# Optimization experiments

Measured on AMD Instinct MI355X. Metric: run time of the kernel, lower is better.

The kernel has to match this reference:

```python
import jax, jax.numpy as jnp
import numpy as np

DIM = 512
NUM_HEADS = 8
HEAD_DIM = DIM // NUM_HEADS
SCALE = HEAD_DIM ** -0.5
B, N = 8, 1024


def setup_inputs() -> dict:
    key = jax.random.key(0)
    k1, k2, k3, k4, k5 = jax.random.split(key, 5)
    x = jax.random.normal(k1, (B, N, DIM), dtype=jnp.float32)
    rpe_bias = jax.random.normal(k2, (1, NUM_HEADS, N, N), dtype=jnp.float32)
    # torch Linear weights: [out_features, in_features], y = x @ W.T
    qkv_w = jax.random.normal(k3, (3 * DIM, DIM), dtype=jnp.float32) * (DIM ** -0.5)
    proj_w = jax.random.normal(k4, (DIM, DIM), dtype=jnp.float32) * (DIM ** -0.5)
    proj_b = jax.random.normal(k5, (DIM,), dtype=jnp.float32) * 0.01
    return {"x": x, "rpe_bias": rpe_bias, "qkv_w": qkv_w, "proj_w": proj_w, "proj_b": proj_b}


def reference(x, rpe_bias, qkv_w, proj_w, proj_b):
    b, n, c = x.shape
    h, d = NUM_HEADS, HEAD_DIM
    # qkv projection (no bias): [B,N,3C] -> [3,B,H,N,D]
    qkv = (x @ qkv_w.T).reshape(b, n, 3, h, d).transpose(2, 0, 3, 1, 4)
    q, k, v = qkv[0], qkv[1], qkv[2]
    attn = jnp.einsum('bhnd,bhmd->bhnm', q, k) * SCALE + rpe_bias
    attn = jax.nn.softmax(attn, axis=-1)  # dropout p=0 -> identity
    out = jnp.einsum('bhnm,bhmd->bhnd', attn, v)
    out = out.transpose(0, 2, 1, 3).reshape(b, n, c)
    return out @ proj_w.T + proj_b
```

## Files before the change

### kernel.cpp

```cpp
#include <hip/hip_runtime.h>
#include <hip/hip_bf16.h>

#define B_    8
#define N_    1024
#define DIM_  512
#define H_    8
#define DH_   64
#define SCALE_ 0.125f

typedef unsigned short u16;
typedef __attribute__((ext_vector_type(8))) short bf16x8;
typedef __attribute__((ext_vector_type(4))) float f32x4;

__device__ __forceinline__ u16 f2bf(float f) {
  union { float f; unsigned u; } v; v.f = f;
  return (u16)((v.u + 0x7fffu + ((v.u >> 16) & 1u)) >> 16);
}
__device__ __forceinline__ unsigned pack2(float a, float b) {
  return (unsigned)f2bf(a) | ((unsigned)f2bf(b) << 16);
}
__device__ __forceinline__ void cp16(const void* g, void* l) {
  __builtin_amdgcn_global_load_lds(
      (const __attribute__((address_space(1))) unsigned*)g,
      (__attribute__((address_space(3))) unsigned*)l, 16, 0, 0);
}

__global__ __launch_bounds__(256) void convert_kernel(
    const float* __restrict__ X, const float* __restrict__ Wq,
    const float* __restrict__ Wp, u16* __restrict__ Xb,
    u16* __restrict__ Wqb, u16* __restrict__ Wpb) {
  const int NX4 = (B_ * N_ * DIM_) / 4;
  const int NQ4 = (3 * DIM_ * DIM_) / 4;
  const int NP4 = (DIM_ * DIM_) / 4;
  const int total = NX4 + NQ4 + NP4;
  const int stride = gridDim.x * 256;
  for (int i = blockIdx.x * 256 + threadIdx.x; i < total; i += stride) {
    const float* s; u16* d; int off;
    if (i < NX4)            { s = X;  d = Xb;  off = i; }
    else if (i < NX4 + NQ4) { s = Wq; d = Wqb; off = i - NX4; }
    else                    { s = Wp; d = Wpb; off = i - NX4 - NQ4; }
    float4 f = *(const float4*)(s + (size_t)off * 4);
    uint2 u; u.x = pack2(f.x, f.y); u.y = pack2(f.z, f.w);
    *(uint2*)(d + (size_t)off * 4) = u;
  }
}

__global__ __launch_bounds__(256) void qkv_gemm(
    const u16* __restrict__ Ab, const u16* __restrict__ Bb,
    u16* __restrict__ Q, u16* __restrict__ K, u16* __restrict__ Vt) {
  __shared__ __align__(16) u16 sA[128 * 64];
  __shared__ __align__(16) u16 sB[128 * 64];
  const int t = threadIdx.x;
  const int wv = t >> 6, lane = t & 63, quad = (lane >> 4) & 3, l15 = lane & 15;
  const int wr = wv >> 1, wc = wv & 1;
  const int m0 = blockIdx.y * 128;
  const int n0 = blockIdx.x * 128;

  const int srow = lane >> 3;
  const int schunk = (lane & 7) ^ srow;
  const size_t ga = (size_t)(m0 + srow) * DIM_ + schunk * 8;
  const size_t gb = (size_t)(n0 + srow) * DIM_ + schunk * 8;

  f32x4 zero = {0.f, 0.f, 0.f, 0.f};
  f32x4 acc[4][4];
#pragma unroll
  for (int i = 0; i < 4; i++)
#pragma unroll
    for (int j = 0; j < 4; j++) acc[i][j] = zero;

  for (int k0 = 0; k0 < DIM_; k0 += 64) {
    __syncthreads();
#pragma unroll
    for (int i = 0; i < 4; i++) {
      const int rb = 32 * wv + 8 * i;
      cp16(Ab + ga + (size_t)rb * DIM_ + k0, &sA[rb * 64]);
      cp16(Bb + gb + (size_t)rb * DIM_ + k0, &sB[rb * 64]);
    }
    __syncthreads();
#pragma unroll
    for (int ks = 0; ks < 2; ks++) {
      bf16x8 af[4], bfv[4];
#pragma unroll
      for (int i = 0; i < 4; i++)
        af[i] = *(const bf16x8*)&sA[(wr * 64 + 16 * i + l15) * 64 +
                                    (((ks << 2) | quad) ^ (l15 & 7)) * 8];
#pragma unroll
      for (int j = 0; j < 4; j++)
        bfv[j] = *(const bf16x8*)&sB[(wc * 64 + 16 * j + l15) * 64 +
                                     (((ks << 2) | quad) ^ (l15 & 7)) * 8];
#pragma unroll
      for (int i = 0; i < 4; i++)
#pragma unroll
        for (int j = 0; j < 4; j++)
          acc[i][j] = __builtin_amdgcn_mfma_f32_16x16x32_bf16(af[i], bfv[j], acc[i][j], 0, 0, 0);
    }
  }

  const int tsel = n0 >> 9;
#pragma unroll
  for (int j = 0; j < 4; j++) {
    const int jg = n0 + wc * 64 + 16 * j + l15;
    const int h = (jg >> 6) & 7, d = jg & 63;
#pragma unroll
    for (int i = 0; i < 4; i++) {
      const int mbase = m0 + wr * 64 + 16 * i + quad * 4;
      const int b = mbase >> 10, nb = mbase & 1023;
      const size_t bh = (size_t)(b * H_ + h);
      if (tsel == 2) {
        ushort4 v4;
        v4.x = f2bf(acc[i][j][0]); v4.y = f2bf(acc[i][j][1]);
        v4.z = f2bf(acc[i][j][2]); v4.w = f2bf(acc[i][j][3]);
        *(ushort4*)&Vt[(bh * DH_ + d) * N_ + nb] = v4;
      } else {
        u16* dst = (tsel == 0 ? Q : K);
#pragma unroll
        for (int rr = 0; rr < 4; rr++)
          dst[(bh * N_ + nb + rr) * DH_ + d] = f2bf(acc[i][j][rr]);
      }
    }
  }
}

__global__ __launch_bounds__(256) void attn_kernel(
    const u16* __restrict__ Q, const u16* __restrict__ K,
    const u16* __restrict__ Vt, const float* __restrict__ bias,
    u16* __restrict__ AO) {
  __shared__ __align__(16) u16 sK[64 * 72];
  __shared__ __align__(16) u16 sV[64 * 72];
  __shared__ __align__(16) u16 sP[64 * 72];
  const int t = threadIdx.x;
  const int wv = t >> 6, lane = t & 63, quad = (lane >> 4) & 3, l15 = lane & 15;

  const int bid = blockIdx.x;
  const int h = bid & 7;
  const int s = bid >> 3;
  const int nx = s >> 3;
  const int b = s & 7;
  const int n0 = nx * 64;
  const int bh = b * H_ + h;
  const int r = t >> 2, c = (t & 3) << 4;

  const int qg = n0 + 16 * wv + l15;
  bf16x8 qf0, qf1;
  {
    const u16* qsrc = Q + (((size_t)bh << 10) + qg) * DH_ + (quad << 3);
    qf0 = *(const bf16x8*)qsrc;
    qf1 = *(const bf16x8*)(qsrc + 32);
  }

  const float* bp = bias + (((size_t)h << 10) + qg) * N_ + (quad << 2);
  const u16* kbase = K + (((size_t)bh << 10) + r) * DH_ + c;
  const u16* vbase = Vt + (((size_t)bh << 6) + r) * N_ + c;

  f32x4 zero = {0.f, 0.f, 0.f, 0.f};
  f32x4 O[4];
  O[0] = zero; O[1] = zero; O[2] = zero; O[3] = zero;
  float lsum = 0.f;

  uint4 kA0 = *(const uint4*)kbase, kA1 = *(const uint4*)(kbase + 8);
  uint4 vA0 = *(const uint4*)vbase, vA1 = *(const uint4*)(vbase + 8);
  uint4 kB0 = *(const uint4*)(kbase + (size_t)64 * DH_);
  uint4 kB1 = *(const uint4*)(kbase + (size_t)64 * DH_ + 8);
  uint4 vB0 = *(const uint4*)(vbase + 64), vB1 = *(const uint4*)(vbase + 72);
  float4 bA[4], bB[4];
#pragma unroll
  for (int cb = 0; cb < 4; cb++) {
    bA[cb] = *(const float4*)(bp + 16 * cb);
    bB[cb] = *(const float4*)(bp + 64 + 16 * cb);
  }

  auto tile = [&](int kt, uint4& k0r, uint4& k1r, uint4& v0r, uint4& v1r,
                  float4 (&bias4)[4]) {
    __syncthreads();
    *(uint4*)&sK[r * 72 + c] = k0r;  *(uint4*)&sK[r * 72 + c + 8] = k1r;
    *(uint4*)&sV[r * 72 + c] = v0r;  *(uint4*)&sV[r * 72 + c + 8] = v1r;
    if (kt + 2 < 16) {
      const u16* kn = kbase + (size_t)(kt + 2) * 64 * DH_;
      const u16* vn = vbase + (kt + 2) * 64;
      k0r = *(const uint4*)kn; k1r = *(const uint4*)(kn + 8);
      v0r = *(const uint4*)vn; v1r = *(const uint4*)(vn + 8);
    }
    __syncthreads();

    f32x4 S[4];
    S[0] = zero; S[1] = zero; S[2] = zero; S[3] = zero;
#pragma unroll
    for (int ks = 0; ks < 2; ks++) {
      const bf16x8 qf = ks ? qf1 : qf0;
#pragma unroll
      for (int cb = 0; cb < 4; cb++) {
        bf16x8 kf = *(const bf16x8*)&sK[(16 * cb + l15) * 72 + ks * 32 + (quad << 3)];
        S[cb] = __builtin_amdgcn_mfma_f32_16x16x32_bf16(kf, qf, S[cb], 0, 0, 0);
      }
    }

#pragma unroll
    for (int cb = 0; cb < 4; cb++) {
      float p0 = __expf(fmaf(S[cb][0], SCALE_, bias4[cb].x));
      float p1 = __expf(fmaf(S[cb][1], SCALE_, bias4[cb].y));
      float p2 = __expf(fmaf(S[cb][2], SCALE_, bias4[cb].z));
      float p3 = __expf(fmaf(S[cb][3], SCALE_, bias4[cb].w));
      lsum += (p0 + p1) + (p2 + p3);
      uint2 pk;
      pk.x = pack2(p0, p1);
      pk.y = pack2(p2, p3);
      *(uint2*)&sP[(16 * wv + l15) * 72 + 16 * cb + (quad << 2)] = pk;
    }
    if (kt + 2 < 16) {
      const float* bn = bp + (kt + 2) * 64;
#pragma unroll
      for (int cb = 0; cb < 4; cb++) bias4[cb] = *(const float4*)(bn + 16 * cb);
    }
    asm volatile("s_waitcnt lgkmcnt(0)" ::: "memory");

#pragma unroll
    for (int ks = 0; ks < 2; ks++) {
      bf16x8 pf = *(const bf16x8*)&sP[(16 * wv + l15) * 72 + ks * 32 + (quad << 3)];
#pragma unroll
      for (int cb = 0; cb < 4; cb++) {
        bf16x8 vf = *(const bf16x8*)&sV[(16 * cb + l15) * 72 + ks * 32 + (quad << 3)];
        O[cb] = __builtin_amdgcn_mfma_f32_16x16x32_bf16(vf, pf, O[cb], 0, 0, 0);
      }
    }
  };

  for (int kt = 0; kt < 16; kt += 2) {
    tile(kt, kA0, kA1, vA0, vA1, bA);
    tile(kt + 1, kB0, kB1, vB0, vB1, bB);
  }

  lsum += __shfl_xor(lsum, 16);
  lsum += __shfl_xor(lsum, 32);
  const float inv = 1.f / lsum;
#pragma unroll
  for (int cb = 0; cb < 4; cb++) {
    ushort4 o4;
    o4.x = f2bf(O[cb][0] * inv); o4.y = f2bf(O[cb][1] * inv);
    o4.z = f2bf(O[cb][2] * inv); o4.w = f2bf(O[cb][3] * inv);
    *(ushort4*)&AO[(((size_t)b << 10) + qg) * DIM_ + h * DH_ + 16 * cb + (quad << 2)] = o4;
  }
}

__global__ __launch_bounds__(256) void proj_gemm(
    const u16* __restrict__ Ab, const u16* __restrict__ Bb,
    const float* __restrict__ Pb, float* __restrict__ Out) {
  __shared__ __align__(16) u16 sA[128 * 64];
  __shared__ __align__(16) u16 sB[128 * 64];
  const int t = threadIdx.x;
  const int wv = t >> 6, lane = t & 63, quad = (lane >> 4) & 3, l15 = lane & 15;
  const int wr = wv >> 1, wc = wv & 1;
  const int m0 = blockIdx.y * 128;
  const int n0 = blockIdx.x * 128;

  const int srow = lane >> 3;
  const int schunk = (lane & 7) ^ srow;
  const size_t ga = (size_t)(m0 + srow) * DIM_ + schunk * 8;
  const size_t gb = (size_t)(n0 + srow) * DIM_ + schunk * 8;

  f32x4 zero = {0.f, 0.f, 0.f, 0.f};
  f32x4 acc[4][4];
#pragma unroll
  for (int i = 0; i < 4; i++)
#pragma unroll
    for (int j = 0; j < 4; j++) acc[i][j] = zero;

  for (int k0 = 0; k0 < DIM_; k0 += 64) {
    __syncthreads();
#pragma unroll
    for (int i = 0; i < 4; i++) {
      const int rb = 32 * wv + 8 * i;
      cp16(Ab + ga + (size_t)rb * DIM_ + k0, &sA[rb * 64]);
      cp16(Bb + gb + (size_t)rb * DIM_ + k0, &sB[rb * 64]);
    }
    __syncthreads();
#pragma unroll
    for (int ks = 0; ks < 2; ks++) {
      bf16x8 af[4], bfv[4];
#pragma unroll
      for (int i = 0; i < 4; i++)
        af[i] = *(const bf16x8*)&sA[(wr * 64 + 16 * i + l15) * 64 +
                                    (((ks << 2) | quad) ^ (l15 & 7)) * 8];
#pragma unroll
      for (int j = 0; j < 4; j++)
        bfv[j] = *(const bf16x8*)&sB[(wc * 64 + 16 * j + l15) * 64 +
                                     (((ks << 2) | quad) ^ (l15 & 7)) * 8];
#pragma unroll
      for (int i = 0; i < 4; i++)
#pragma unroll
        for (int j = 0; j < 4; j++)
          acc[i][j] = __builtin_amdgcn_mfma_f32_16x16x32_bf16(af[i], bfv[j], acc[i][j], 0, 0, 0);
    }
  }

#pragma unroll
  for (int j = 0; j < 4; j++) {
    const int jg = n0 + wc * 64 + 16 * j + l15;
    const float pb = Pb[jg];
#pragma unroll
    for (int i = 0; i < 4; i++) {
      const int mbase = m0 + wr * 64 + 16 * i + quad * 4;
#pragma unroll
      for (int rr = 0; rr < 4; rr++)
        Out[(size_t)(mbase + rr) * DIM_ + jg] = acc[i][j][rr] + pb;
    }
  }
}

extern "C" void kernel_launch(void* const* d_in, const int* in_sizes, int n_in,
                              void* d_out, int out_size, void* d_ws, size_t ws_size,
                              hipStream_t stream) {
  const float* x      = (const float*)d_in[0];
  const float* rpe    = (const float*)d_in[1];
  const float* qkv_w  = (const float*)d_in[2];
  const float* proj_w = (const float*)d_in[3];
  const float* proj_b = (const float*)d_in[4];
  float* out = (float*)d_out;

  const size_t perbuf = (size_t)B_ * N_ * DIM_;
  u16* Xb  = (u16*)d_ws;
  u16* Q   = Xb + perbuf;
  u16* K   = Q + perbuf;
  u16* Vt  = K + perbuf;
  u16* Wqb = Vt + perbuf;
  u16* Wpb = Wqb + (size_t)3 * DIM_ * DIM_;
  u16* AO  = Xb;

  convert_kernel<<<2560, 256, 0, stream>>>(x, qkv_w, proj_w, Xb, Wqb, Wpb);
  qkv_gemm<<<dim3(12, 64), 256, 0, stream>>>(Xb, Wqb, Q, K, Vt);
  attn_kernel<<<1024, 256, 0, stream>>>(Q, K, Vt, rpe, AO);
  proj_gemm<<<dim3(4, 64), 256, 0, stream>>>(AO, Wpb, proj_b, out);
}
```

Measured before the change: 182.2 us.

## Process two 64-row query tiles per attention block to reuse K/V tiles

Each attention block now covers 128 query rows as two 64-row halves, so every K/V tile staged in shared memory is used twice. The grid halves to 512 blocks. K and V fragments are held in registers across both halves, and the two-tile prefetch double buffer becomes a single-tile prefetch with bias loaded per iteration. This cuts shared-memory staging and global K/V traffic per query, at the cost of more registers, fewer blocks for 256 CUs, and less latency hiding for bias loads.

```diff
diff --git a/kernel.cpp b/kernel.cpp
--- a/kernel.cpp
+++ b/kernel.cpp
@@ -136,108 +136,135 @@
   const int s = bid >> 3;
   const int nx = s >> 3;
   const int b = s & 7;
-  const int n0 = nx * 64;
+  const int n0 = nx << 7;
   const int bh = b * H_ + h;
   const int r = t >> 2, c = (t & 3) << 4;
 
-  const int qg = n0 + 16 * wv + l15;
-  bf16x8 qf0, qf1;
+  const int qgA = n0 + 16 * wv + l15;
+  const int qgB = qgA + 64;
+  bf16x8 qfA0, qfA1, qfB0, qfB1;
   {
-    const u16* qsrc = Q + (((size_t)bh << 10) + qg) * DH_ + (quad << 3);
-    qf0 = *(const bf16x8*)qsrc;
-    qf1 = *(const bf16x8*)(qsrc + 32);
-  }
-
-  const float* bp = bias + (((size_t)h << 10) + qg) * N_ + (quad << 2);
+    const u16* qa = Q + (((size_t)bh << 10) + qgA) * DH_ + (quad << 3);
+    const u16* qb = Q + (((size_t)bh << 10) + qgB) * DH_ + (quad << 3);
+    qfA0 = *(const bf16x8*)qa; qfA1 = *(const bf16x8*)(qa + 32);
+    qfB0 = *(const bf16x8*)qb; qfB1 = *(const bf16x8*)(qb + 32);
+  }
+
+  const float* bpA = bias + (((size_t)h << 10) + qgA) * N_ + (quad << 2);
+  const float* bpB = bias + (((size_t)h << 10) + qgB) * N_ + (quad << 2);
   const u16* kbase = K + (((size_t)bh << 10) + r) * DH_ + c;
   const u16* vbase = Vt + (((size_t)bh << 6) + r) * N_ + c;
 
   f32x4 zero = {0.f, 0.f, 0.f, 0.f};
-  f32x4 O[4];
-  O[0] = zero; O[1] = zero; O[2] = zero; O[3] = zero;
-  float lsum = 0.f;
-
-  uint4 kA0 = *(const uint4*)kbase, kA1 = *(const uint4*)(kbase + 8);
-  uint4 vA0 = *(const uint4*)vbase, vA1 = *(const uint4*)(vbase + 8);
-  uint4 kB0 = *(const uint4*)(kbase + (size_t)64 * DH_);
-  uint4 kB1 = *(const uint4*)(kbase + (size_t)64 * DH_ + 8);
-  uint4 vB0 = *(const uint4*)(vbase + 64), vB1 = *(const uint4*)(vbase + 72);
-  float4 bA[4], bB[4];
-#pragma unroll
-  for (int cb = 0; cb < 4; cb++) {
-    bA[cb] = *(const float4*)(bp + 16 * cb);
-    bB[cb] = *(const float4*)(bp + 64 + 16 * cb);
-  }
-
-  auto tile = [&](int kt, uint4& k0r, uint4& k1r, uint4& v0r, uint4& v1r,
-                  float4 (&bias4)[4]) {
+  f32x4 OA[4], OB[4];
+#pragma unroll
+  for (int i = 0; i < 4; i++) { OA[i] = zero; OB[i] = zero; }
+  float lsumA = 0.f, lsumB = 0.f;
+
+  uint4 k0r = *(const uint4*)kbase, k1r = *(const uint4*)(kbase + 8);
+  uint4 v0r = *(const uint4*)vbase, v1r = *(const uint4*)(vbase + 8);
+
+  for (int kt = 0; kt < 16; kt++) {
+    const int m0k = kt << 6;
     __syncthreads();
     *(uint4*)&sK[r * 72 + c] = k0r;  *(uint4*)&sK[r * 72 + c + 8] = k1r;
     *(uint4*)&sV[r * 72 + c] = v0r;  *(uint4*)&sV[r * 72 + c + 8] = v1r;
-    if (kt + 2 < 16) {
-      const u16* kn = kbase + (size_t)(kt + 2) * 64 * DH_;
-      const u16* vn = vbase + (kt + 2) * 64;
+    if (kt < 15) {
+      const u16* kn = kbase + (size_t)(kt + 1) * 64 * DH_;
+      const u16* vn = vbase + (kt + 1) * 64;
       k0r = *(const uint4*)kn; k1r = *(const uint4*)(kn + 8);
       v0r = *(const uint4*)vn; v1r = *(const uint4*)(vn + 8);
     }
-    __syncthreads();
-
-    f32x4 S[4];
-    S[0] = zero; S[1] = zero; S[2] = zero; S[3] = zero;
-#pragma unroll
-    for (int ks = 0; ks < 2; ks++) {
-      const bf16x8 qf = ks ? qf1 : qf0;
+    float4 bA[4], bB[4];
+#pragma unroll
+    for (int cb = 0; cb < 4; cb++) {
+      bA[cb] = *(const float4*)(bpA + m0k + 16 * cb);
+      bB[cb] = *(const float4*)(bpB + m0k + 16 * cb);
+    }
+    __syncthreads();
+
+    bf16x8 kf[8];
+#pragma unroll
+    for (int ks = 0; ks < 2; ks++)
+#pragma unroll
+      for (int cb = 0; cb < 4; cb++)
+        kf[ks * 4 + cb] =
+            *(const bf16x8*)&sK[(16 * cb + l15) * 72 + ks * 32 + (quad << 3)];
+
+    f32x4 SA[4], SB[4];
+#pragma unroll
+    for (int i = 0; i < 4; i++) { SA[i] = zero; SB[i] = zero; }
+#pragma unroll
+    for (int ks = 0; ks < 2; ks++) {
+      const bf16x8 qa = ks ? qfA1 : qfA0;
+      const bf16x8 qb = ks ? qfB1 : qfB0;
 #pragma unroll
       for (int cb = 0; cb < 4; cb++) {
-        bf16x8 kf = *(const bf16x8*)&sK[(16 * cb + l15) * 72 + ks * 32 + (quad << 3)];
-        S[cb] = __builtin_amdgcn_mfma_f32_16x16x32_bf16(kf, qf, S[cb], 0, 0, 0);
+        SA[cb] = __builtin_amdgcn_mfma_f32_16x16x32_bf16(kf[ks * 4 + cb], qa, SA[cb], 0, 0, 0);
+        SB[cb] = __builtin_amdgcn_mfma_f32_16x16x32_bf16(kf[ks * 4 + cb], qb, SB[cb], 0, 0, 0);
       }
     }
 
 #pragma unroll
     for (int cb = 0; cb < 4; cb++) {
-      float p0 = __expf(fmaf(S[cb][0], SCALE_, bias4[cb].x));
-      float p1 = __expf(fmaf(S[cb][1], SCALE_, bias4[cb].y));
-      float p2 = __expf(fmaf(S[cb][2], SCALE_, bias4[cb].z));
-      float p3 = __expf(fmaf(S[cb][3], SCALE_, bias4[cb].w));
-      lsum += (p0 + p1) + (p2 + p3);
-      uint2 pk;
-      pk.x = pack2(p0, p1);
-      pk.y = pack2(p2, p3);
+      float p0 = __expf(fmaf(SA[cb][0], SCALE_, bA[cb].x));
+      float p1 = __expf(fmaf(SA[cb][1], SCALE_, bA[cb].y));
+      float p2 = __expf(fmaf(SA[cb][2], SCALE_, bA[cb].z));
+      float p3 = __expf(fmaf(SA[cb][3], SCALE_, bA[cb].w));
+      lsumA += (p0 + p1) + (p2 + p3);
+      uint2 pk; pk.x = pack2(p0, p1); pk.y = pack2(p2, p3);
       *(uint2*)&sP[(16 * wv + l15) * 72 + 16 * cb + (quad << 2)] = pk;
     }
-    if (kt + 2 < 16) {
-      const float* bn = bp + (kt + 2) * 64;
-#pragma unroll
-      for (int cb = 0; cb < 4; cb++) bias4[cb] = *(const float4*)(bn + 16 * cb);
-    }
+    bf16x8 vf[8];
+#pragma unroll
+    for (int ks = 0; ks < 2; ks++)
+#pragma unroll
+      for (int cb = 0; cb < 4; cb++)
+        vf[ks * 4 + cb] =
+            *(const bf16x8*)&sV[(16 * cb + l15) * 72 + ks * 32 + (quad << 3)];
     asm volatile("s_waitcnt lgkmcnt(0)" ::: "memory");
 
 #pragma unroll
     for (int ks = 0; ks < 2; ks++) {
       bf16x8 pf = *(const bf16x8*)&sP[(16 * wv + l15) * 72 + ks * 32 + (quad << 3)];
 #pragma unroll
-      for (int cb = 0; cb < 4; cb++) {
-        bf16x8 vf = *(const bf16x8*)&sV[(16 * cb + l15) * 72 + ks * 32 + (quad << 3)];
-        O[cb] = __builtin_amdgcn_mfma_f32_16x16x32_bf16(vf, pf, O[cb], 0, 0, 0);
-      }
-    }
-  };
-
-  for (int kt = 0; kt < 16; kt += 2) {
-    tile(kt, kA0, kA1, vA0, vA1, bA);
-    tile(kt + 1, kB0, kB1, vB0, vB1, bB);
-  }
-
-  lsum += __shfl_xor(lsum, 16);
-  lsum += __shfl_xor(lsum, 32);
-  const float inv = 1.f / lsum;
+      for (int cb = 0; cb < 4; cb++)
+        OA[cb] = __builtin_amdgcn_mfma_f32_16x16x32_bf16(vf[ks * 4 + cb], pf, OA[cb], 0, 0, 0);
+    }
+
+#pragma unroll
+    for (int cb = 0; cb < 4; cb++) {
+      float p0 = __expf(fmaf(SB[cb][0], SCALE_, bB[cb].x));
+      float p1 = __expf(fmaf(SB[cb][1], SCALE_, bB[cb].y));
+      float p2 = __expf(fmaf(SB[cb][2], SCALE_, bB[cb].z));
+      float p3 = __expf(fmaf(SB[cb][3], SCALE_, bB[cb].w));
+      lsumB += (p0 + p1) + (p2 + p3);
+      uint2 pk; pk.x = pack2(p0, p1); pk.y = pack2(p2, p3);
+      *(uint2*)&sP[(16 * wv + l15) * 72 + 16 * cb + (quad << 2)] = pk;
+    }
+    asm volatile("s_waitcnt lgkmcnt(0)" ::: "memory");
+#pragma unroll
+    for (int ks = 0; ks < 2; ks++) {
+      bf16x8 pf = *(const bf16x8*)&sP[(16 * wv + l15) * 72 + ks * 32 + (quad << 3)];
+#pragma unroll
+      for (int cb = 0; cb < 4; cb++)
+        OB[cb] = __builtin_amdgcn_mfma_f32_16x16x32_bf16(vf[ks * 4 + cb], pf, OB[cb], 0, 0, 0);
+    }
+  }
+
+  lsumA += __shfl_xor(lsumA, 16); lsumA += __shfl_xor(lsumA, 32);
+  lsumB += __shfl_xor(lsumB, 16); lsumB += __shfl_xor(lsumB, 32);
+  const float invA = 1.f / lsumA, invB = 1.f / lsumB;
 #pragma unroll
   for (int cb = 0; cb < 4; cb++) {
     ushort4 o4;
-    o4.x = f2bf(O[cb][0] * inv); o4.y = f2bf(O[cb][1] * inv);
-    o4.z = f2bf(O[cb][2] * inv); o4.w = f2bf(O[cb][3] * inv);
-    *(ushort4*)&AO[(((size_t)b << 10) + qg) * DIM_ + h * DH_ + 16 * cb + (quad << 2)] = o4;
+    o4.x = f2bf(OA[cb][0] * invA); o4.y = f2bf(OA[cb][1] * invA);
+    o4.z = f2bf(OA[cb][2] * invA); o4.w = f2bf(OA[cb][3] * invA);
+    *(ushort4*)&AO[(((size_t)b << 10) + qgA) * DIM_ + h * DH_ + 16 * cb + (quad << 2)] = o4;
+    ushort4 p4;
+    p4.x = f2bf(OB[cb][0] * invB); p4.y = f2bf(OB[cb][1] * invB);
+    p4.z = f2bf(OB[cb][2] * invB); p4.w = f2bf(OB[cb][3] * invB);
+    *(ushort4*)&AO[(((size_t)b << 10) + qgB) * DIM_ + h * DH_ + 16 * cb + (quad << 2)] = p4;
   }
 }
 
@@ -327,6 +354,6 @@
 
   convert_kernel<<<2560, 256, 0, stream>>>(x, qkv_w, proj_w, Xb, Wqb, Wpb);
   qkv_gemm<<<dim3(12, 64), 256, 0, stream>>>(Xb, Wqb, Q, K, Vt);
-  attn_kernel<<<1024, 256, 0, stream>>>(Q, K, Vt, rpe, AO);
+  attn_kernel<<<512, 256, 0, stream>>>(Q, K, Vt, rpe, AO);
   proj_gemm<<<dim3(4, 64), 256, 0, stream>>>(AO, Wpb, proj_b, out);
 }
```

Measured after the change: 174.6 us. 4.2% less time.
